# Kernel optimization log

Measured on AMD Instinct MI355X. Metric: run time of the kernel, lower is better.

## Reference

```python
import jax, jax.numpy as jnp
import numpy as np

NOPE = 128          # qk_nope_head_dim
ROPE = 64           # qk_rope_head_dim
KV_LORA = 512       # kv_lora_rank
SCALE = (KV_LORA + ROPE) ** (-0.5)


def setup_inputs() -> dict:
    key = jax.random.key(0)
    k1, k2, k3, k4, k5 = jax.random.split(key, 5)
    T, H, K, S = 512, 128, 512, 8192
    q = jax.random.normal(k1, (T, H, NOPE + ROPE), dtype=jnp.float32)
    kv_cache = jax.random.normal(k2, (S, KV_LORA + ROPE), dtype=jnp.float32)
    topk_indices = jax.random.randint(k3, (T, K), 0, S, dtype=jnp.int32)
    k_b_proj_trans = jax.random.normal(k4, (H, KV_LORA, NOPE), dtype=jnp.float32) * 0.02
    v_b_proj = jax.random.normal(k5, (H, 128, KV_LORA), dtype=jnp.float32) * 0.02
    return {"q": q, "kv_cache": kv_cache, "topk_indices": topk_indices,
            "k_b_proj_trans": k_b_proj_trans, "v_b_proj": v_b_proj}


def reference(q, kv_cache, topk_indices, k_b_proj_trans, v_b_proj):
    # q: [T, H, 192]; kv_cache: [S, 576]; topk_indices: [T, K]
    q_nope, q_rope = q[..., :NOPE], q[..., NOPE:]
    # bmm_out(q_nope_t, k_b_proj_trans.transpose(1,2)): [T,H,128] x [H,512,128] -> [T,H,512]
    q_lat = jnp.einsum('thd,hkd->thk', q_nope, k_b_proj_trans)
    q_concat = jnp.concatenate([q_lat, q_rope], axis=-1)        # [T, H, 576]
    # sparse MLA: gather selected latent KV per token
    kv_sel = kv_cache[topk_indices]                              # [T, K, 576]
    scores = jnp.einsum('thc,tkc->thk', q_concat, kv_sel) * SCALE
    p = jax.nn.softmax(scores, axis=-1)                          # [T, H, K]
    attn_lat = jnp.einsum('thk,tkc->thc', p, kv_sel[..., :KV_LORA])  # [T, H, 512]
    # bmm_out(attn_lat_t, v_b_proj.transpose(1,2)): [T,H,512] x [H,512,128] -> [T,H,128]
    out = jnp.einsum('thc,hvc->thv', attn_lat, v_b_proj)
    return out
```

## Files before the change

kernel.cpp:

```cpp
#include <hip/hip_runtime.h>
#include <stdint.h>


#define SCALE 0.041666666666666664f

typedef __bf16 bf16x8 __attribute__((ext_vector_type(8)));
typedef float floatx4 __attribute__((ext_vector_type(4)));

static __device__ __forceinline__ unsigned short f2bf(float f) {
  unsigned int u = __builtin_bit_cast(unsigned int, f);
  u += 0x7FFF + ((u >> 16) & 1);
  return (unsigned short)(u >> 16);
}
static __device__ __forceinline__ float bf2f(unsigned short h) {
  unsigned int u = ((unsigned int)h) << 16;
  return __builtin_bit_cast(float, u);
}
static __device__ __forceinline__ unsigned int pack2(float lo, float hi) {
  return (unsigned int)f2bf(lo) | ((unsigned int)f2bf(hi) << 16);
}
static __device__ __forceinline__ void stage8_f32(const float* __restrict__ src,
                                                  unsigned short* dst) {
  const float4* s4 = reinterpret_cast<const float4*>(src);
  float4 v0 = s4[0], v1 = s4[1];
  uint4 o;
  o.x = pack2(v0.x, v0.y); o.y = pack2(v0.z, v0.w);
  o.z = pack2(v1.x, v1.y); o.w = pack2(v1.z, v1.w);
  *reinterpret_cast<uint4*>(dst) = o;
}
static __device__ __forceinline__ void stage8_bf(const unsigned short* __restrict__ src,
                                                 unsigned short* dst) {
  *reinterpret_cast<uint4*>(dst) = *reinterpret_cast<const uint4*>(src);
}

static __device__ __forceinline__ void mfma_4x4_s(const unsigned short* As,
                                                  const unsigned short* Bs,
                                                  int wm, int wn, int l15, int quad,
                                                  int bstride, floatx4 acc[4][4]) {
  bf16x8 af[4], bfr[4];
#pragma unroll
  for (int i = 0; i < 4; ++i)
    af[i] = *reinterpret_cast<const bf16x8*>(&As[(wm + i * 16 + l15) * 32 + quad * 8]);
#pragma unroll
  for (int j = 0; j < 4; ++j)
    bfr[j] = *reinterpret_cast<const bf16x8*>(&Bs[(wn + j * 16 + l15) * bstride + quad * 8]);
#pragma unroll
  for (int i = 0; i < 4; ++i)
#pragma unroll
    for (int j = 0; j < 4; ++j)
      acc[i][j] = __builtin_amdgcn_mfma_f32_16x16x32_bf16(af[i], bfr[j], acc[i][j], 0, 0, 0);
}
static __device__ __forceinline__ void mfma_4x4(const unsigned short* As,
                                                const unsigned short* Bs,
                                                int wm, int wn, int l15, int quad,
                                                floatx4 acc[4][4]) {
  mfma_4x4_s(As, Bs, wm, wn, l15, quad, 32, acc);
}

__global__ void kv_convert(const float* __restrict__ kv, unsigned short* __restrict__ kvb) {
  int i = blockIdx.x * 256 + threadIdx.x;
  float4 v = reinterpret_cast<const float4*>(kv)[i];
  ushort4 o;
  o.x = f2bf(v.x); o.y = f2bf(v.y); o.z = f2bf(v.z); o.w = f2bf(v.w);
  reinterpret_cast<ushort4*>(kvb)[i] = o;
}

__global__ void rope_copy(const float* __restrict__ q, unsigned short* __restrict__ qc) {
  int i = blockIdx.x * 256 + threadIdx.x;
  int r = i & 63;
  int th = i >> 6;
  qc[(size_t)th * 576 + 512 + r] = f2bf(q[(size_t)th * 192 + 128 + r] * SCALE);
}

__global__ __launch_bounds__(256) void qlat_gemm(const float* __restrict__ q,
                                                 const float* __restrict__ kb,
                                                 unsigned short* __restrict__ qc) {
  const int h = blockIdx.y;
  const int tm = (blockIdx.x & 3) * 128;
  const int tn = (blockIdx.x >> 2) * 128;
  __shared__ __align__(16) unsigned short As[128 * 32];
  __shared__ __align__(16) unsigned short Bs[128 * 32];
  const int tid = threadIdx.x;
  const int lane = tid & 63, wave = tid >> 6;
  const int wm = (wave & 1) * 64, wn = (wave >> 1) * 64;
  const int l15 = lane & 15, quad = lane >> 4;
  const int r0 = tid >> 2, cg = tid & 3;
  const float* a0 = q + ((size_t)(tm + r0) * 128 + h) * 192 + cg * 8;
  const float* a1 = q + ((size_t)(tm + r0 + 64) * 128 + h) * 192 + cg * 8;
  const float* b0 = kb + ((size_t)h * 512 + tn + r0) * 128 + cg * 8;
  const float* b1 = b0 + (size_t)64 * 128;
  floatx4 acc[4][4] = {};
  for (int ks = 0; ks < 4; ++ks) {
    stage8_f32(a0 + ks * 32, &As[r0 * 32 + cg * 8]);
    stage8_f32(a1 + ks * 32, &As[(r0 + 64) * 32 + cg * 8]);
    stage8_f32(b0 + ks * 32, &Bs[r0 * 32 + cg * 8]);
    stage8_f32(b1 + ks * 32, &Bs[(r0 + 64) * 32 + cg * 8]);
    __syncthreads();
    mfma_4x4(As, Bs, wm, wn, l15, quad, acc);
    __syncthreads();
  }
#pragma unroll
  for (int i = 0; i < 4; ++i) {
    const int row = wm + i * 16 + quad * 4;
#pragma unroll
    for (int j = 0; j < 4; ++j) {
      const int col = wn + j * 16 + l15;
#pragma unroll
      for (int r = 0; r < 4; ++r) {
        const int t = tm + row + r;
        qc[((size_t)t * 128 + h) * 576 + tn + col] = f2bf(acc[i][j][r] * SCALE);
      }
    }
  }
}

__global__ __launch_bounds__(256) void scores_gemm(const unsigned short* __restrict__ qc,
                                                   const unsigned short* __restrict__ kvb,
                                                   const int* __restrict__ topk,
                                                   unsigned short* __restrict__ P) {
  const int t = blockIdx.y;
  const int tn = blockIdx.x * 128;
  __shared__ __align__(16) unsigned short As[128 * 32];
  __shared__ __align__(16) unsigned short Bs[128 * 32];
  const int tid = threadIdx.x;
  const int lane = tid & 63, wave = tid >> 6;
  const int wm = (wave & 1) * 64, wn = (wave >> 1) * 64;
  const int l15 = lane & 15, quad = lane >> 4;
  const int r0 = tid >> 2, cg = tid & 3;
  const unsigned short* a0 = qc + ((size_t)t * 128 + r0) * 576 + cg * 8;
  const unsigned short* a1 = a0 + (size_t)64 * 576;
  const int idx0 = topk[t * 512 + tn + r0];
  const int idx1 = topk[t * 512 + tn + r0 + 64];
  const unsigned short* b0 = kvb + (size_t)idx0 * 576 + cg * 8;
  const unsigned short* b1 = kvb + (size_t)idx1 * 576 + cg * 8;
  floatx4 acc[4][4] = {};
  for (int ks = 0; ks < 18; ++ks) {
    stage8_bf(a0 + ks * 32, &As[r0 * 32 + cg * 8]);
    stage8_bf(a1 + ks * 32, &As[(r0 + 64) * 32 + cg * 8]);
    stage8_bf(b0 + ks * 32, &Bs[r0 * 32 + cg * 8]);
    stage8_bf(b1 + ks * 32, &Bs[(r0 + 64) * 32 + cg * 8]);
    __syncthreads();
    mfma_4x4(As, Bs, wm, wn, l15, quad, acc);
    __syncthreads();
  }
#pragma unroll
  for (int i = 0; i < 4; ++i) {
    const int row = wm + i * 16 + quad * 4;
#pragma unroll
    for (int j = 0; j < 4; ++j) {
      const int col = tn + wn + j * 16 + l15;
#pragma unroll
      for (int r = 0; r < 4; ++r)
        P[((size_t)t * 128 + row + r) * 512 + col] = f2bf(acc[i][j][r]);
    }
  }
}

__global__ __launch_bounds__(256) void softmax_rows(unsigned short* __restrict__ P) {
  const int row = blockIdx.x * 4 + (threadIdx.x >> 6);
  const int lane = threadIdx.x & 63;
  unsigned short* rp = P + (size_t)row * 512 + lane * 8;
  uint4 raw = *reinterpret_cast<const uint4*>(rp);
  unsigned int w[4] = {raw.x, raw.y, raw.z, raw.w};
  float f[8];
  float mx = -1e30f;
#pragma unroll
  for (int i = 0; i < 8; ++i) {
    f[i] = bf2f((unsigned short)((w[i >> 1] >> ((i & 1) * 16)) & 0xFFFF));
    mx = fmaxf(mx, f[i]);
  }
#pragma unroll
  for (int off = 32; off; off >>= 1) mx = fmaxf(mx, __shfl_xor(mx, off, 64));
  float s = 0.f;
#pragma unroll
  for (int i = 0; i < 8; ++i) { f[i] = __expf(f[i] - mx); s += f[i]; }
#pragma unroll
  for (int off = 32; off; off >>= 1) s += __shfl_xor(s, off, 64);
  const float inv = 1.0f / s;
  uint4 o;
  o.x = pack2(f[0] * inv, f[1] * inv);
  o.y = pack2(f[2] * inv, f[3] * inv);
  o.z = pack2(f[4] * inv, f[5] * inv);
  o.w = pack2(f[6] * inv, f[7] * inv);
  *reinterpret_cast<uint4*>(rp) = o;
}

#define BSTRIDE 40
__global__ __launch_bounds__(256) void attn_gemm(const unsigned short* __restrict__ P,
                                                 const unsigned short* __restrict__ kvb,
                                                 const int* __restrict__ topk,
                                                 unsigned short* __restrict__ alat) {
  const int t = blockIdx.y;
  const int tn = blockIdx.x * 128;
  __shared__ __align__(16) unsigned short As[128 * 32];
  __shared__ __align__(16) unsigned short St[32 * 128];
  __shared__ __align__(16) unsigned short Bs[128 * BSTRIDE];
  const int tid = threadIdx.x;
  const int lane = tid & 63, wave = tid >> 6;
  const int wm = (wave & 1) * 64, wn = (wave >> 1) * 64;
  const int l15 = lane & 15, quad = lane >> 4;
  const int r0 = tid >> 2, cg = tid & 3;
  const unsigned short* a0 = P + ((size_t)t * 128 + r0) * 512 + cg * 8;
  const unsigned short* a1 = a0 + (size_t)64 * 512;
  const int key0 = tid >> 4;
  const int cs = tid & 15;
  const int* tkrow = topk + t * 512;
  floatx4 acc[4][4] = {};
  for (int ks = 0; ks < 16; ++ks) {
    stage8_bf(a0 + ks * 32, &As[r0 * 32 + cg * 8]);
    stage8_bf(a1 + ks * 32, &As[(r0 + 64) * 32 + cg * 8]);
    {
      const int i0 = tkrow[ks * 32 + key0];
      const int i1 = tkrow[ks * 32 + key0 + 16];
      *reinterpret_cast<uint4*>(&St[key0 * 128 + cs * 8]) =
          *reinterpret_cast<const uint4*>(kvb + (size_t)i0 * 576 + tn + cs * 8);
      *reinterpret_cast<uint4*>(&St[(key0 + 16) * 128 + cs * 8]) =
          *reinterpret_cast<const uint4*>(kvb + (size_t)i1 * 576 + tn + cs * 8);
    }
    __syncthreads();
#pragma unroll
    for (int it = 0; it < 2; ++it) {
      const int p = it * 256 + tid;
      const int c = p & 127;
      const int kg = p >> 7;
      unsigned short tmp[8];
#pragma unroll
      for (int i = 0; i < 8; ++i) tmp[i] = St[(kg * 8 + i) * 128 + c];
      *reinterpret_cast<uint4*>(&Bs[c * BSTRIDE + kg * 8]) =
          *reinterpret_cast<const uint4*>(tmp);
    }
    __syncthreads();
    mfma_4x4_s(As, Bs, wm, wn, l15, quad, BSTRIDE, acc);
    __syncthreads();
  }
#pragma unroll
  for (int i = 0; i < 4; ++i) {
    const int row = wm + i * 16 + quad * 4;
#pragma unroll
    for (int j = 0; j < 4; ++j) {
      const int col = tn + wn + j * 16 + l15;
#pragma unroll
      for (int r = 0; r < 4; ++r)
        alat[((size_t)(row + r) * 512 + t) * 512 + col] = f2bf(acc[i][j][r]);
    }
  }
}

__global__ __launch_bounds__(256) void out_gemm(const unsigned short* __restrict__ alat,
                                                const float* __restrict__ vb,
                                                float* __restrict__ out) {
  const int h = blockIdx.y;
  const int tm = blockIdx.x * 128;
  __shared__ __align__(16) unsigned short As[128 * 32];
  __shared__ __align__(16) unsigned short Bs[128 * 32];
  const int tid = threadIdx.x;
  const int lane = tid & 63, wave = tid >> 6;
  const int wm = (wave & 1) * 64, wn = (wave >> 1) * 64;
  const int l15 = lane & 15, quad = lane >> 4;
  const int r0 = tid >> 2, cg = tid & 3;
  const unsigned short* a0 = alat + ((size_t)h * 512 + tm + r0) * 512 + cg * 8;
  const unsigned short* a1 = a0 + (size_t)64 * 512;
  const float* b0 = vb + ((size_t)h * 128 + r0) * 512 + cg * 8;
  const float* b1 = b0 + (size_t)64 * 512;
  floatx4 acc[4][4] = {};
  for (int ks = 0; ks < 16; ++ks) {
    stage8_bf(a0 + ks * 32, &As[r0 * 32 + cg * 8]);
    stage8_bf(a1 + ks * 32, &As[(r0 + 64) * 32 + cg * 8]);
    stage8_f32(b0 + ks * 32, &Bs[r0 * 32 + cg * 8]);
    stage8_f32(b1 + ks * 32, &Bs[(r0 + 64) * 32 + cg * 8]);
    __syncthreads();
    mfma_4x4(As, Bs, wm, wn, l15, quad, acc);
    __syncthreads();
  }
#pragma unroll
  for (int i = 0; i < 4; ++i) {
    const int row = wm + i * 16 + quad * 4;
#pragma unroll
    for (int j = 0; j < 4; ++j) {
      const int col = wn + j * 16 + l15;
#pragma unroll
      for (int r = 0; r < 4; ++r) {
        const int t = tm + row + r;
        out[((size_t)t * 128 + h) * 128 + col] = acc[i][j][r];
      }
    }
  }
}

extern "C" void kernel_launch(void* const* d_in, const int* in_sizes, int n_in,
                              void* d_out, int out_size, void* d_ws, size_t ws_size,
                              hipStream_t stream) {
  const float* q = (const float*)d_in[0];
  const float* kv = (const float*)d_in[1];
  const int* topk = (const int*)d_in[2];
  const float* kb = (const float*)d_in[3];
  const float* vb = (const float*)d_in[4];
  float* out = (float*)d_out;

  char* ws = (char*)d_ws;
  unsigned short* kvb = (unsigned short*)ws;
  unsigned short* qc = (unsigned short*)(ws + 9437184);
  unsigned short* alat = qc;
  unsigned short* P = (unsigned short*)(ws + 9437184 + 75497472);

  kv_convert<<<dim3(4608), dim3(256), 0, stream>>>(kv, kvb);
  rope_copy<<<dim3(16384), dim3(256), 0, stream>>>(q, qc);
  qlat_gemm<<<dim3(16, 128), dim3(256), 0, stream>>>(q, kb, qc);
  scores_gemm<<<dim3(4, 512), dim3(256), 0, stream>>>(qc, kvb, topk, P);
  softmax_rows<<<dim3(16384), dim3(256), 0, stream>>>(P);
  attn_gemm<<<dim3(4, 512), dim3(256), 0, stream>>>(P, kvb, topk, alat);
  out_gemm<<<dim3(4, 128), dim3(256), 0, stream>>>(alat, vb, out);
}
```

Measured before the change: 402.7 us.

## Use direct global-to-LDS DMA loads and swap grid dimension order in GEMMs

Replaces register-staged global→shared copies of bf16 tiles with global_load_lds 16-byte DMA in the scores, attn and out GEMMs, so data no longer passes through VGPRs. The LDS destination index becomes tid*8, which matches the old r0*32+cg*8 layout for the first 64 rows. The grid axes are also swapped so consecutive blocks walk over heads/tokens instead of N-tiles, which changes L2 locality. The risk is that the 16-byte LDS DMA variant may be unsupported or behave differently on this hardware, and the changed scheduling could reduce cache reuse of shared tiles.

```diff
diff --git a/kernel.cpp b/kernel.cpp
--- a/kernel.cpp
+++ b/kernel.cpp
@@ -18,6 +18,11 @@
 }
 static __device__ __forceinline__ unsigned int pack2(float lo, float hi) {
   return (unsigned int)f2bf(lo) | ((unsigned int)f2bf(hi) << 16);
+}
+static __device__ __forceinline__ void ldsdma16(const void* g, void* l) {
+  __builtin_amdgcn_global_load_lds(
+      (const __attribute__((address_space(1))) void*)g,
+      (__attribute__((address_space(3))) void*)l, 16, 0, 0);
 }
 static __device__ __forceinline__ void stage8_f32(const float* __restrict__ src,
                                                   unsigned short* dst) {
@@ -75,9 +80,9 @@
 __global__ __launch_bounds__(256) void qlat_gemm(const float* __restrict__ q,
                                                  const float* __restrict__ kb,
                                                  unsigned short* __restrict__ qc) {
-  const int h = blockIdx.y;
-  const int tm = (blockIdx.x & 3) * 128;
-  const int tn = (blockIdx.x >> 2) * 128;
+  const int h = blockIdx.x;
+  const int tm = (blockIdx.y & 3) * 128;
+  const int tn = (blockIdx.y >> 2) * 128;
   __shared__ __align__(16) unsigned short As[128 * 32];
   __shared__ __align__(16) unsigned short Bs[128 * 32];
   const int tid = threadIdx.x;
@@ -91,10 +96,10 @@
   const float* b1 = b0 + (size_t)64 * 128;
   floatx4 acc[4][4] = {};
   for (int ks = 0; ks < 4; ++ks) {
-    stage8_f32(a0 + ks * 32, &As[r0 * 32 + cg * 8]);
-    stage8_f32(a1 + ks * 32, &As[(r0 + 64) * 32 + cg * 8]);
-    stage8_f32(b0 + ks * 32, &Bs[r0 * 32 + cg * 8]);
-    stage8_f32(b1 + ks * 32, &Bs[(r0 + 64) * 32 + cg * 8]);
+    stage8_f32(a0 + ks * 32, &As[tid * 8]);
+    stage8_f32(a1 + ks * 32, &As[2048 + tid * 8]);
+    stage8_f32(b0 + ks * 32, &Bs[tid * 8]);
+    stage8_f32(b1 + ks * 32, &Bs[2048 + tid * 8]);
     __syncthreads();
     mfma_4x4(As, Bs, wm, wn, l15, quad, acc);
     __syncthreads();
@@ -118,8 +123,8 @@
                                                    const unsigned short* __restrict__ kvb,
                                                    const int* __restrict__ topk,
                                                    unsigned short* __restrict__ P) {
-  const int t = blockIdx.y;
-  const int tn = blockIdx.x * 128;
+  const int t = blockIdx.x;
+  const int tn = blockIdx.y * 128;
   __shared__ __align__(16) unsigned short As[128 * 32];
   __shared__ __align__(16) unsigned short Bs[128 * 32];
   const int tid = threadIdx.x;
@@ -135,10 +140,10 @@
   const unsigned short* b1 = kvb + (size_t)idx1 * 576 + cg * 8;
   floatx4 acc[4][4] = {};
   for (int ks = 0; ks < 18; ++ks) {
-    stage8_bf(a0 + ks * 32, &As[r0 * 32 + cg * 8]);
-    stage8_bf(a1 + ks * 32, &As[(r0 + 64) * 32 + cg * 8]);
-    stage8_bf(b0 + ks * 32, &Bs[r0 * 32 + cg * 8]);
-    stage8_bf(b1 + ks * 32, &Bs[(r0 + 64) * 32 + cg * 8]);
+    ldsdma16(a0 + ks * 32, &As[tid * 8]);
+    ldsdma16(a1 + ks * 32, &As[2048 + tid * 8]);
+    ldsdma16(b0 + ks * 32, &Bs[tid * 8]);
+    ldsdma16(b1 + ks * 32, &Bs[2048 + tid * 8]);
     __syncthreads();
     mfma_4x4(As, Bs, wm, wn, l15, quad, acc);
     __syncthreads();
@@ -190,8 +195,8 @@
                                                  const unsigned short* __restrict__ kvb,
                                                  const int* __restrict__ topk,
                                                  unsigned short* __restrict__ alat) {
-  const int t = blockIdx.y;
-  const int tn = blockIdx.x * 128;
+  const int t = blockIdx.x;
+  const int tn = blockIdx.y * 128;
   __shared__ __align__(16) unsigned short As[128 * 32];
   __shared__ __align__(16) unsigned short St[32 * 128];
   __shared__ __align__(16) unsigned short Bs[128 * BSTRIDE];
@@ -199,24 +204,19 @@
   const int lane = tid & 63, wave = tid >> 6;
   const int wm = (wave & 1) * 64, wn = (wave >> 1) * 64;
   const int l15 = lane & 15, quad = lane >> 4;
-  const int r0 = tid >> 2, cg = tid & 3;
-  const unsigned short* a0 = P + ((size_t)t * 128 + r0) * 512 + cg * 8;
+  const unsigned short* a0 = P + ((size_t)t * 128 + (tid >> 2)) * 512 + (tid & 3) * 8;
   const unsigned short* a1 = a0 + (size_t)64 * 512;
   const int key0 = tid >> 4;
   const int cs = tid & 15;
   const int* tkrow = topk + t * 512;
   floatx4 acc[4][4] = {};
   for (int ks = 0; ks < 16; ++ks) {
-    stage8_bf(a0 + ks * 32, &As[r0 * 32 + cg * 8]);
-    stage8_bf(a1 + ks * 32, &As[(r0 + 64) * 32 + cg * 8]);
-    {
-      const int i0 = tkrow[ks * 32 + key0];
-      const int i1 = tkrow[ks * 32 + key0 + 16];
-      *reinterpret_cast<uint4*>(&St[key0 * 128 + cs * 8]) =
-          *reinterpret_cast<const uint4*>(kvb + (size_t)i0 * 576 + tn + cs * 8);
-      *reinterpret_cast<uint4*>(&St[(key0 + 16) * 128 + cs * 8]) =
-          *reinterpret_cast<const uint4*>(kvb + (size_t)i1 * 576 + tn + cs * 8);
-    }
+    ldsdma16(a0 + ks * 32, &As[tid * 8]);
+    ldsdma16(a1 + ks * 32, &As[2048 + tid * 8]);
+    const int i0 = tkrow[ks * 32 + key0];
+    const int i1 = tkrow[ks * 32 + key0 + 16];
+    ldsdma16(kvb + (size_t)i0 * 576 + tn + cs * 8, &St[tid * 8]);
+    ldsdma16(kvb + (size_t)i1 * 576 + tn + cs * 8, &St[2048 + tid * 8]);
     __syncthreads();
 #pragma unroll
     for (int it = 0; it < 2; ++it) {
@@ -249,8 +249,8 @@
 __global__ __launch_bounds__(256) void out_gemm(const unsigned short* __restrict__ alat,
                                                 const float* __restrict__ vb,
                                                 float* __restrict__ out) {
-  const int h = blockIdx.y;
-  const int tm = blockIdx.x * 128;
+  const int h = blockIdx.x;
+  const int tm = blockIdx.y * 128;
   __shared__ __align__(16) unsigned short As[128 * 32];
   __shared__ __align__(16) unsigned short Bs[128 * 32];
   const int tid = threadIdx.x;
@@ -264,10 +264,10 @@
   const float* b1 = b0 + (size_t)64 * 512;
   floatx4 acc[4][4] = {};
   for (int ks = 0; ks < 16; ++ks) {
-    stage8_bf(a0 + ks * 32, &As[r0 * 32 + cg * 8]);
-    stage8_bf(a1 + ks * 32, &As[(r0 + 64) * 32 + cg * 8]);
-    stage8_f32(b0 + ks * 32, &Bs[r0 * 32 + cg * 8]);
-    stage8_f32(b1 + ks * 32, &Bs[(r0 + 64) * 32 + cg * 8]);
+    ldsdma16(a0 + ks * 32, &As[tid * 8]);
+    ldsdma16(a1 + ks * 32, &As[2048 + tid * 8]);
+    stage8_f32(b0 + ks * 32, &Bs[tid * 8]);
+    stage8_f32(b1 + ks * 32, &Bs[2048 + tid * 8]);
     __syncthreads();
     mfma_4x4(As, Bs, wm, wn, l15, quad, acc);
     __syncthreads();
@@ -305,9 +305,9 @@
 
   kv_convert<<<dim3(4608), dim3(256), 0, stream>>>(kv, kvb);
   rope_copy<<<dim3(16384), dim3(256), 0, stream>>>(q, qc);
-  qlat_gemm<<<dim3(16, 128), dim3(256), 0, stream>>>(q, kb, qc);
-  scores_gemm<<<dim3(4, 512), dim3(256), 0, stream>>>(qc, kvb, topk, P);
+  qlat_gemm<<<dim3(128, 16), dim3(256), 0, stream>>>(q, kb, qc);
+  scores_gemm<<<dim3(512, 4), dim3(256), 0, stream>>>(qc, kvb, topk, P);
   softmax_rows<<<dim3(16384), dim3(256), 0, stream>>>(P);
-  attn_gemm<<<dim3(4, 512), dim3(256), 0, stream>>>(P, kvb, topk, alat);
-  out_gemm<<<dim3(4, 128), dim3(256), 0, stream>>>(alat, vb, out);
-}
+  attn_gemm<<<dim3(512, 4), dim3(256), 0, stream>>>(P, kvb, topk, alat);
+  out_gemm<<<dim3(128, 4), dim3(256), 0, stream>>>(alat, vb, out);
+}
```

Result: no change. 400.0 us (-0.7%).
